# Optimization experiments

Hardware: AMD Instinct MI355X
Metric: run time of the kernel (lower is better)

## Reference

```python
import jax, jax.numpy as jnp
import numpy as np

B, N, F_IN = 1, 4096, 128
H, F_OUT = 8, 64
NEG = -1e9


def setup_inputs() -> dict:
    key = jax.random.key(0)
    ks = jax.random.split(key, 7)
    x = jax.random.normal(ks[0], (B, N, F_IN), dtype=jnp.float32)
    edge = jax.random.uniform(ks[1], (N, N)) < 0.02
    edge = edge | jnp.eye(N, dtype=bool)
    adj = jnp.where(edge, 0.0, NEG).astype(jnp.float32)
    # Glorot-uniform params
    def glorot(k, shape, fan_in, fan_out):
        lim = float(np.sqrt(6.0 / (fan_in + fan_out)))
        return jax.random.uniform(k, shape, jnp.float32, -lim, lim)
    W_proj = glorot(ks[2], (H * F_OUT, F_IN), F_IN, H * F_OUT)      # linear_proj.weight
    a_src = glorot(ks[3], (1, H, F_OUT), H, F_OUT)                   # scoring_fn_source
    a_tgt = glorot(ks[4], (1, H, F_OUT), H, F_OUT)                   # scoring_fn_target
    W_skip = glorot(ks[5], (H * F_OUT, F_IN), F_IN, H * F_OUT)       # skip_proj.weight
    bias = jnp.zeros((H * F_OUT,), dtype=jnp.float32)
    return {"in_nodes_features": x, "adj": adj, "W_proj": W_proj,
            "a_src": a_src, "a_tgt": a_tgt, "W_skip": W_skip, "bias": bias}


def reference(in_nodes_features, adj, W_proj, a_src, a_tgt, W_skip, bias):
    x = in_nodes_features                                  # [B,N,Fin]  (dropout p=0)
    proj = jnp.einsum('bnf,of->bno', x, W_proj)            # [B,N,H*Fo]
    proj = proj.reshape(B, N, H, F_OUT)                    # [B,N,H,Fo]
    s_src = jnp.einsum('bnhd,xhd->bhn', proj, a_src)       # [B,H,N] (row / source)
    s_tgt = jnp.einsum('bnhd,xhd->bhn', proj, a_tgt)       # [B,H,N] (col / target)
    scores = s_src[:, :, :, None] + s_tgt[:, :, None, :]   # [B,H,N,N]
    scores = jax.nn.leaky_relu(scores, negative_slope=0.2)
    att = jax.nn.softmax(scores + adj, axis=-1)            # adj additive mask, broadcast over B,H
    out = jnp.einsum('bhij,bjhd->bihd', att, proj)         # [B,N,H,Fo]
    out = out + jnp.einsum('bnf,of->bno', x, W_skip).reshape(B, N, H, F_OUT)  # skip (dims differ)
    out = out.reshape(B, N, H * F_OUT) + bias              # concat + bias
    out = jax.nn.elu(out)                                  # activation ELU
    return out, adj
```

## Files before the change

### kernel.cpp

```cpp
#include <hip/hip_runtime.h>
#include <cmath>

#define N_NODES 4096
#define FIN     128
#define H_HEADS 8
#define FOUT    64
#define HF      512
#define CAP     256

typedef float  vf4 __attribute__((ext_vector_type(4)));
typedef unsigned int vu4 __attribute__((ext_vector_type(4)));

__device__ __forceinline__ unsigned short f2bf(float f) {
    unsigned u = __float_as_uint(f);
    u += 0x7fff + ((u >> 16) & 1);
    return (unsigned short)(u >> 16);
}

__global__ __launch_bounds__(256) void gemm_fused(
    const float* __restrict__ x, const float* __restrict__ Wp,
    const float* __restrict__ Ws, const float* __restrict__ a_src,
    const float* __restrict__ a_tgt,
    unsigned short* __restrict__ proj, float* __restrict__ skip,
    float* __restrict__ ssrc, float* __restrict__ stgt)
{
    __shared__ __align__(16) float AsT[64][68];
    __shared__ __align__(16) float BsT[64][68];

    const int t  = threadIdx.x;
    const int rb = blockIdx.y * 64;
    const int cb = blockIdx.x * 64;
    const bool isP = (cb < HF);
    const float* Wbase = isP ? (Wp + cb * FIN) : (Ws + (cb - HF) * FIN);

    const int tx = t & 15;
    const int ty = t >> 4;
    float acc[4][4] = {{0.f}};

    for (int kb = 0; kb < FIN; kb += 64) {
        #pragma unroll
        for (int p = 0; p < 4; ++p) {
            int f4 = t + p * 256;
            int r  = f4 >> 4;
            int k4 = f4 & 15;
            float4 a = *(const float4*)(x + (size_t)(rb + r) * FIN + kb + k4 * 4);
            AsT[k4*4+0][r] = a.x; AsT[k4*4+1][r] = a.y;
            AsT[k4*4+2][r] = a.z; AsT[k4*4+3][r] = a.w;
            float4 b = *(const float4*)(Wbase + (size_t)r * FIN + kb + k4 * 4);
            BsT[k4*4+0][r] = b.x; BsT[k4*4+1][r] = b.y;
            BsT[k4*4+2][r] = b.z; BsT[k4*4+3][r] = b.w;
        }
        __syncthreads();
        #pragma unroll 8
        for (int kk = 0; kk < 64; ++kk) {
            float4 a = *(const float4*)&AsT[kk][ty * 4];
            float4 b = *(const float4*)&BsT[kk][tx * 4];
            acc[0][0] += a.x*b.x; acc[0][1] += a.x*b.y; acc[0][2] += a.x*b.z; acc[0][3] += a.x*b.w;
            acc[1][0] += a.y*b.x; acc[1][1] += a.y*b.y; acc[1][2] += a.y*b.z; acc[1][3] += a.y*b.w;
            acc[2][0] += a.z*b.x; acc[2][1] += a.z*b.y; acc[2][2] += a.z*b.z; acc[2][3] += a.z*b.w;
            acc[3][0] += a.w*b.x; acc[3][1] += a.w*b.y; acc[3][2] += a.w*b.z; acc[3][3] += a.w*b.w;
        }
        __syncthreads();
    }

    if (isP) {
        #pragma unroll
        for (int i = 0; i < 4; ++i) {
            ushort4 v;
            v.x = f2bf(acc[i][0]); v.y = f2bf(acc[i][1]);
            v.z = f2bf(acc[i][2]); v.w = f2bf(acc[i][3]);
            *(ushort4*)(proj + (size_t)(rb + ty*4 + i) * HF + cb + tx * 4) = v;
        }
        const int h = cb >> 6;
        const float as0 = a_src[cb + tx*4 + 0], as1 = a_src[cb + tx*4 + 1];
        const float as2 = a_src[cb + tx*4 + 2], as3 = a_src[cb + tx*4 + 3];
        const float at0 = a_tgt[cb + tx*4 + 0], at1 = a_tgt[cb + tx*4 + 1];
        const float at2 = a_tgt[cb + tx*4 + 2], at3 = a_tgt[cb + tx*4 + 3];
        #pragma unroll
        for (int i = 0; i < 4; ++i) {
            float ps = acc[i][0]*as0 + acc[i][1]*as1 + acc[i][2]*as2 + acc[i][3]*as3;
            float pt = acc[i][0]*at0 + acc[i][1]*at1 + acc[i][2]*at2 + acc[i][3]*at3;
            #pragma unroll
            for (int off = 1; off < 16; off <<= 1) {
                ps += __shfl_xor(ps, off);
                pt += __shfl_xor(pt, off);
            }
            if (tx == 0) {
                int n = rb + ty*4 + i;
                ssrc[n * H_HEADS + h] = ps;
                stgt[n * H_HEADS + h] = pt;
            }
        }
    } else {
        #pragma unroll
        for (int i = 0; i < 4; ++i) {
            float4 v = make_float4(acc[i][0], acc[i][1], acc[i][2], acc[i][3]);
            *(float4*)(skip + (size_t)(rb + ty*4 + i) * HF + (cb - HF) + tx * 4) = v;
        }
    }
}

__global__ __launch_bounds__(512) void att_kernel(
    const float* __restrict__ adj, const unsigned short* __restrict__ proj,
    const float* __restrict__ skip, const float* __restrict__ ssrc,
    const float* __restrict__ stgt, const float* __restrict__ bias,
    float* __restrict__ out, float* __restrict__ adj_out)
{
    __shared__ int   s_idx[CAP];
    __shared__ float sp[H_HEADS][CAP];
    __shared__ float s_i[H_HEADS];
    __shared__ int   s_cnt;

    const int t = threadIdx.x;
    const int i = blockIdx.x;
    if (t == 0) s_cnt = 0;
    if (t < H_HEADS) s_i[t] = ssrc[i * H_HEADS + t];
    __syncthreads();

    const vf4* arow = (const vf4*)(adj + (size_t)i * N_NODES);
    vf4*       aout = (vf4*)(adj_out + (size_t)i * N_NODES);
    #pragma unroll
    for (int it = 0; it < 2; ++it) {
        int f4 = t + it * 512;
        vf4 v = __builtin_nontemporal_load(arow + f4);
        __builtin_nontemporal_store(v, aout + f4);
        int j0 = f4 * 4;
        if (v.x == 0.0f) { int p = atomicAdd(&s_cnt, 1); if (p < CAP) s_idx[p] = j0;     }
        if (v.y == 0.0f) { int p = atomicAdd(&s_cnt, 1); if (p < CAP) s_idx[p] = j0 + 1; }
        if (v.z == 0.0f) { int p = atomicAdd(&s_cnt, 1); if (p < CAP) s_idx[p] = j0 + 2; }
        if (v.w == 0.0f) { int p = atomicAdd(&s_cnt, 1); if (p < CAP) s_idx[p] = j0 + 3; }
    }
    __syncthreads();
    const int c = (s_cnt < CAP) ? s_cnt : CAP;

    for (int k = t; k < c; k += 512) {
        int j = s_idx[k];
        const float* st = stgt + j * H_HEADS;
        float4 t0 = *(const float4*)(st);
        float4 t1 = *(const float4*)(st + 4);
        float e;
        e = s_i[0] + t0.x; sp[0][k] = (e > 0.f) ? e : 0.2f * e;
        e = s_i[1] + t0.y; sp[1][k] = (e > 0.f) ? e : 0.2f * e;
        e = s_i[2] + t0.z; sp[2][k] = (e > 0.f) ? e : 0.2f * e;
        e = s_i[3] + t0.w; sp[3][k] = (e > 0.f) ? e : 0.2f * e;
        e = s_i[4] + t1.x; sp[4][k] = (e > 0.f) ? e : 0.2f * e;
        e = s_i[5] + t1.y; sp[5][k] = (e > 0.f) ? e : 0.2f * e;
        e = s_i[6] + t1.z; sp[6][k] = (e > 0.f) ? e : 0.2f * e;
        e = s_i[7] + t1.w; sp[7][k] = (e > 0.f) ? e : 0.2f * e;
    }
    __syncthreads();

    const int h    = t >> 6;
    const int lane = t & 63;
    float m = -1e30f;
    for (int k = lane; k < c; k += 64) m = fmaxf(m, sp[h][k]);
    #pragma unroll
    for (int off = 32; off; off >>= 1) m = fmaxf(m, __shfl_xor(m, off));
    float l = 0.0f;
    for (int k = lane; k < c; k += 64) {
        float e = __expf(sp[h][k] - m);
        sp[h][k] = e;
        l += e;
    }
    #pragma unroll
    for (int off = 32; off; off >>= 1) l += __shfl_xor(l, off);
    const float inv = 1.0f / l;

    const int g  = lane >> 3;
    const int k8 = lane & 7;
    float a8[8] = {0.f, 0.f, 0.f, 0.f, 0.f, 0.f, 0.f, 0.f};
    const unsigned short* pbase = proj + h * FOUT + k8 * 8;
    #pragma unroll 2
    for (int k = g; k < c; k += 8) {
        int   j = s_idx[k];
        float p = sp[h][k];
        vu4 raw = *(const vu4*)(pbase + (size_t)j * HF);
        a8[0] += p * __uint_as_float(raw.x << 16);
        a8[1] += p * __uint_as_float(raw.x & 0xffff0000u);
        a8[2] += p * __uint_as_float(raw.y << 16);
        a8[3] += p * __uint_as_float(raw.y & 0xffff0000u);
        a8[4] += p * __uint_as_float(raw.z << 16);
        a8[5] += p * __uint_as_float(raw.z & 0xffff0000u);
        a8[6] += p * __uint_as_float(raw.w << 16);
        a8[7] += p * __uint_as_float(raw.w & 0xffff0000u);
    }
    #pragma unroll
    for (int off = 8; off < 64; off <<= 1) {
        #pragma unroll
        for (int q = 0; q < 8; ++q) a8[q] += __shfl_xor(a8[q], off);
    }
    if (g == 0) {
        const int o = h * FOUT + k8 * 8;
        const float* sk = skip + (size_t)i * HF + o;
        const float* bs = bias + o;
        float r[8];
        #pragma unroll
        for (int q = 0; q < 8; ++q) {
            float v = a8[q] * inv + sk[q] + bs[q];
            r[q] = (v > 0.f) ? v : expm1f(v);
        }
        float4 w0 = make_float4(r[0], r[1], r[2], r[3]);
        float4 w1 = make_float4(r[4], r[5], r[6], r[7]);
        *(float4*)(out + (size_t)i * HF + o)     = w0;
        *(float4*)(out + (size_t)i * HF + o + 4) = w1;
    }
}

extern "C" void kernel_launch(void* const* d_in, const int* in_sizes, int n_in,
                              void* d_out, int out_size, void* d_ws, size_t ws_size,
                              hipStream_t stream)
{
    const float* x     = (const float*)d_in[0];
    const float* adj   = (const float*)d_in[1];
    const float* Wp    = (const float*)d_in[2];
    const float* a_src = (const float*)d_in[3];
    const float* a_tgt = (const float*)d_in[4];
    const float* Ws    = (const float*)d_in[5];
    const float* bias  = (const float*)d_in[6];

    float* out     = (float*)d_out;
    float* adj_out = out + (size_t)N_NODES * HF;

    unsigned short* proj = (unsigned short*)d_ws;
    float* ssrc = (float*)((char*)d_ws + (size_t)N_NODES * HF * sizeof(unsigned short));
    float* stgt = ssrc + (size_t)N_NODES * H_HEADS;
    float* skip = out;

    gemm_fused<<<dim3(16, 64), 256, 0, stream>>>(x, Wp, Ws, a_src, a_tgt,
                                                 proj, skip, ssrc, stgt);
    att_kernel<<<N_NODES, 512, 0, stream>>>(adj, proj, skip, ssrc, stgt, bias,
                                            out, adj_out);
}
```

Measured before the change: 193.9 us.

## Use wave ballot compaction for neighbor list and defer adj copy store

Replaces per-element LDS atomicAdd neighbor compaction with wave-level ballots, popcount prefix offsets and a single atomic per wave. The neighbor index is stored pre-scaled as a byte offset, which removes the multiplies when gathering proj and stgt rows. Accumulation uses packed float2 vectors, which may map to packed FMA. The adj passthrough store is moved to the end of the kernel so it overlaps with other work, at the cost of holding the loaded values in registers for longer.

```diff
diff --git a/kernel.cpp b/kernel.cpp
--- a/kernel.cpp
+++ b/kernel.cpp
@@ -9,6 +9,7 @@
 #define CAP     256
 
 typedef float  vf4 __attribute__((ext_vector_type(4)));
+typedef float  vf2 __attribute__((ext_vector_type(2)));
 typedef unsigned int vu4 __attribute__((ext_vector_type(4)));
 
 __device__ __forceinline__ unsigned short f2bf(float f) {
@@ -111,31 +112,40 @@
     __shared__ float s_i[H_HEADS];
     __shared__ int   s_cnt;
 
-    const int t = threadIdx.x;
-    const int i = blockIdx.x;
+    const int t    = threadIdx.x;
+    const int i    = blockIdx.x;
+    const int lane = t & 63;
     if (t == 0) s_cnt = 0;
     if (t < H_HEADS) s_i[t] = ssrc[i * H_HEADS + t];
     __syncthreads();
 
     const vf4* arow = (const vf4*)(adj + (size_t)i * N_NODES);
-    vf4*       aout = (vf4*)(adj_out + (size_t)i * N_NODES);
+    vf4 va[2];
+    const unsigned long long lt = (1ull << lane) - 1ull;
     #pragma unroll
     for (int it = 0; it < 2; ++it) {
-        int f4 = t + it * 512;
+        const int f4 = t + it * 512;
         vf4 v = __builtin_nontemporal_load(arow + f4);
-        __builtin_nontemporal_store(v, aout + f4);
-        int j0 = f4 * 4;
-        if (v.x == 0.0f) { int p = atomicAdd(&s_cnt, 1); if (p < CAP) s_idx[p] = j0;     }
-        if (v.y == 0.0f) { int p = atomicAdd(&s_cnt, 1); if (p < CAP) s_idx[p] = j0 + 1; }
-        if (v.z == 0.0f) { int p = atomicAdd(&s_cnt, 1); if (p < CAP) s_idx[p] = j0 + 2; }
-        if (v.w == 0.0f) { int p = atomicAdd(&s_cnt, 1); if (p < CAP) s_idx[p] = j0 + 3; }
+        va[it] = v;
+        const int jb = (f4 * 4) << 10;
+        const bool h0 = (v.x == 0.f), h1 = (v.y == 0.f), h2 = (v.z == 0.f), h3 = (v.w == 0.f);
+        const unsigned long long b0 = __ballot(h0), b1 = __ballot(h1);
+        const unsigned long long b2 = __ballot(h2), b3 = __ballot(h3);
+        const int n0 = __popcll(b0), n1 = __popcll(b1), n2 = __popcll(b2);
+        const int total = n0 + n1 + n2 + __popcll(b3);
+        int base = 0;
+        if (lane == 0 && total) base = atomicAdd(&s_cnt, total);
+        base = __shfl(base, 0);
+        if (h0) { int p = base + __popcll(b0 & lt);                if (p < CAP) s_idx[p] = jb;        }
+        if (h1) { int p = base + n0 + __popcll(b1 & lt);           if (p < CAP) s_idx[p] = jb + 1024; }
+        if (h2) { int p = base + n0 + n1 + __popcll(b2 & lt);      if (p < CAP) s_idx[p] = jb + 2048; }
+        if (h3) { int p = base + n0 + n1 + n2 + __popcll(b3 & lt); if (p < CAP) s_idx[p] = jb + 3072; }
     }
     __syncthreads();
     const int c = (s_cnt < CAP) ? s_cnt : CAP;
 
     for (int k = t; k < c; k += 512) {
-        int j = s_idx[k];
-        const float* st = stgt + j * H_HEADS;
+        const float* st = (const float*)((const char*)stgt + (s_idx[k] >> 5));
         float4 t0 = *(const float4*)(st);
         float4 t1 = *(const float4*)(st + 4);
         float e;
@@ -150,8 +160,7 @@
     }
     __syncthreads();
 
-    const int h    = t >> 6;
-    const int lane = t & 63;
+    const int h = t >> 6;
     float m = -1e30f;
     for (int k = lane; k < c; k += 64) m = fmaxf(m, sp[h][k]);
     #pragma unroll
@@ -168,22 +177,22 @@
 
     const int g  = lane >> 3;
     const int k8 = lane & 7;
-    float a8[8] = {0.f, 0.f, 0.f, 0.f, 0.f, 0.f, 0.f, 0.f};
-    const unsigned short* pbase = proj + h * FOUT + k8 * 8;
+    vf2 a2[4] = {{0.f, 0.f}, {0.f, 0.f}, {0.f, 0.f}, {0.f, 0.f}};
+    const char* pbase = (const char*)proj + h * FOUT * 2 + k8 * 16;
     #pragma unroll 2
     for (int k = g; k < c; k += 8) {
-        int   j = s_idx[k];
-        float p = sp[h][k];
-        vu4 raw = *(const vu4*)(pbase + (size_t)j * HF);
-        a8[0] += p * __uint_as_float(raw.x << 16);
-        a8[1] += p * __uint_as_float(raw.x & 0xffff0000u);
-        a8[2] += p * __uint_as_float(raw.y << 16);
-        a8[3] += p * __uint_as_float(raw.y & 0xffff0000u);
-        a8[4] += p * __uint_as_float(raw.z << 16);
-        a8[5] += p * __uint_as_float(raw.z & 0xffff0000u);
-        a8[6] += p * __uint_as_float(raw.w << 16);
-        a8[7] += p * __uint_as_float(raw.w & 0xffff0000u);
-    }
+        const int   off = s_idx[k];
+        const float p   = sp[h][k];
+        const vf2   p2  = {p, p};
+        vu4 raw = *(const vu4*)(pbase + off);
+        vf2 v0 = { __uint_as_float(raw.x << 16), __uint_as_float(raw.x & 0xffff0000u) };
+        vf2 v1 = { __uint_as_float(raw.y << 16), __uint_as_float(raw.y & 0xffff0000u) };
+        vf2 v2 = { __uint_as_float(raw.z << 16), __uint_as_float(raw.z & 0xffff0000u) };
+        vf2 v3 = { __uint_as_float(raw.w << 16), __uint_as_float(raw.w & 0xffff0000u) };
+        a2[0] += p2 * v0; a2[1] += p2 * v1; a2[2] += p2 * v2; a2[3] += p2 * v3;
+    }
+    float a8[8] = {a2[0].x, a2[0].y, a2[1].x, a2[1].y,
+                   a2[2].x, a2[2].y, a2[3].x, a2[3].y};
     #pragma unroll
     for (int off = 8; off < 64; off <<= 1) {
         #pragma unroll
@@ -199,11 +208,13 @@
             float v = a8[q] * inv + sk[q] + bs[q];
             r[q] = (v > 0.f) ? v : expm1f(v);
         }
-        float4 w0 = make_float4(r[0], r[1], r[2], r[3]);
-        float4 w1 = make_float4(r[4], r[5], r[6], r[7]);
-        *(float4*)(out + (size_t)i * HF + o)     = w0;
-        *(float4*)(out + (size_t)i * HF + o + 4) = w1;
-    }
+        *(float4*)(out + (size_t)i * HF + o)     = make_float4(r[0], r[1], r[2], r[3]);
+        *(float4*)(out + (size_t)i * HF + o + 4) = make_float4(r[4], r[5], r[6], r[7]);
+    }
+
+    vf4* aout = (vf4*)(adj_out + (size_t)i * N_NODES);
+    __builtin_nontemporal_store(va[0], aout + t);
+    __builtin_nontemporal_store(va[1], aout + t + 512);
 }
 
 extern "C" void kernel_launch(void* const* d_in, const int* in_sizes, int n_in,
```

After: 191.8 us. No clear change (-1.0%).
